# Performance work log

Hardware: AMD Instinct MI355X
Metric: run time of the kernel (lower is better)

The kernel has to match this reference:

```python
import jax, jax.numpy as jnp
import numpy as np

N = 8192
F_IN = 256
F_OUT = 64
ALPHA = 0.2  # LeakyReLU negative slope
MASK_VAL = -9e15


def setup_inputs() -> dict:
    key = jax.random.key(0)
    k1, k2, k3, k4 = jax.random.split(key, 4)
    h = jax.random.normal(k1, (N, F_IN), dtype=jnp.float32)
    adj = jax.random.randint(k2, (N, N), 0, 2, dtype=jnp.int32)  # 0/1 dense adjacency
    # Parameters (original creates them inside forward with xavier init; here fixed inputs)
    W = jax.random.normal(k3, (F_IN, F_OUT), dtype=jnp.float32) * (1.414 * np.sqrt(2.0 / (F_IN + F_OUT)))
    a = jax.random.normal(k4, (2 * F_OUT, 1), dtype=jnp.float32) * (1.414 * np.sqrt(2.0 / (2 * F_OUT + 1)))
    return {"h": h, "adj": adj, "W": W, "a": a}


def reference(h, adj, W, a):
    # Wh: [N, F_OUT]
    Wh = h @ W
    # e_ij = LeakyReLU(a^T [Wh_i ; Wh_j]) computed via broadcast instead of the
    f_src = Wh @ a[:F_OUT, 0]   # [N] contribution of row node i
    f_dst = Wh @ a[F_OUT:, 0]   # [N] contribution of col node j
    e = jax.nn.leaky_relu(f_src[:, None] + f_dst[None, :], negative_slope=ALPHA)  # [N, N]
    # adj-masked row softmax
    scores = jnp.where(adj > 0, e, MASK_VAL)
    attention = jax.nn.softmax(scores, axis=1)
    # dropout omitted (deterministic eval reference)
    h_prime = attention @ Wh  # [N, F_OUT]
    return jax.nn.elu(h_prime)  # concat=True branch
```

## Files before the change

kernel.cpp:

```cpp
#include <hip/hip_runtime.h>
#include <hip/hip_bf16.h>

#define NN 8192
#define FIN 256
#define FOUT 64
#define L2E 1.4426950408889634f
#define PADK 40

typedef __attribute__((ext_vector_type(8))) short short8;
typedef __attribute__((ext_vector_type(4))) float f32x4;
typedef __attribute__((ext_vector_type(4))) int   iv4;

#define BAR() do { \
  __asm__ __volatile__("s_waitcnt lgkmcnt(0)" ::: "memory"); \
  __builtin_amdgcn_s_barrier(); \
  __asm__ __volatile__("" ::: "memory"); \
} while (0)

__device__ __forceinline__ unsigned short f2bf(float x){
  unsigned u = __float_as_uint(x);
  u += 0x7FFFu + ((u >> 16) & 1u);
  return (unsigned short)(u >> 16);
}

__global__ __launch_bounds__(256) void k_pm(const float* __restrict__ h,
    const float* __restrict__ W, const float* __restrict__ a,
    const int* __restrict__ adj, unsigned short* __restrict__ WhT,
    float* __restrict__ fs, float* __restrict__ fd,
    unsigned* __restrict__ gmax_u, unsigned* __restrict__ mask){
  __shared__ float Ws[128*64];
  __shared__ float hs[8][128];
  const int bid = blockIdx.x, t = threadIdx.x;
  if (bid < 1024){
    const int l = t & 63, wv = t >> 6;
    const int rb = bid * 8;
    float acc0 = 0.f, acc1 = 0.f;
    for (int half = 0; half < 2; ++half){
      if (half) __syncthreads();
      for (int i = t; i < 2048; i += 256)
        ((float4*)Ws)[i] = ((const float4*)W)[half*2048 + i];
      {
        int rr = t >> 5, cc = t & 31;
        ((float4*)&hs[rr][0])[cc] =
            *(const float4*)(h + (size_t)(rb+rr)*FIN + half*128 + cc*4);
      }
      __syncthreads();
      #pragma unroll 8
      for (int k = 0; k < 128; ++k){
        float wval = Ws[k*64 + l];
        acc0 = fmaf(hs[wv*2+0][k], wval, acc0);
        acc1 = fmaf(hs[wv*2+1][k], wval, acc1);
      }
    }
    const int r0 = rb + wv*2, r1 = r0 + 1;
    float a1 = a[l], a2 = a[64 + l];
    float p0 = acc0*a1, q0 = acc0*a2, p1 = acc1*a1, q1 = acc1*a2;
    #pragma unroll
    for (int m = 1; m < 64; m <<= 1){
      p0 += __shfl_xor(p0, m); q0 += __shfl_xor(q0, m);
      p1 += __shfl_xor(p1, m); q1 += __shfl_xor(q1, m);
    }
    if (l == 0){
      fs[r0] = p0*L2E; fs[r1] = p1*L2E; fd[r0] = q0*L2E; fd[r1] = q1*L2E;
      atomicMax(gmax_u, __float_as_uint(q0*L2E + 64.0f));
      atomicMax(gmax_u, __float_as_uint(q1*L2E + 64.0f));
    }
    WhT[(size_t)l*NN + r0] = f2bf(acc0);
    WhT[(size_t)l*NN + r1] = f2bf(acc1);
  } else {
    unsigned char* nib = (unsigned char*)Ws;
    const unsigned b2 = (unsigned)(bid - 1024);
    #pragma unroll 1
    for (int it = 0; it < 16; ++it){
      const unsigned jb = (b2*16u + (unsigned)it) * 2048u;
      const iv4* p = (const iv4*)(adj + jb + (unsigned)t*8u);
      iv4 A = __builtin_nontemporal_load(p);
      iv4 B = __builtin_nontemporal_load(p + 1);
      unsigned by = (unsigned)(A.x!=0)        | ((unsigned)(A.y!=0)<<1)
                  | ((unsigned)(A.z!=0)<<2)   | ((unsigned)(A.w!=0)<<3)
                  | ((unsigned)(B.x!=0)<<4)   | ((unsigned)(B.y!=0)<<5)
                  | ((unsigned)(B.z!=0)<<6)   | ((unsigned)(B.w!=0)<<7);
      if (it) __syncthreads();
      nib[t] = (unsigned char)by;
      __syncthreads();
      if (t < 64) mask[(jb >> 5) + t] = ((const unsigned*)nib)[t];
    }
  }
}

__device__ __forceinline__ void attn_math(unsigned mbits, f32x4 fv0, f32x4 fv1,
    short8 w0, short8 w1, short8 w2, short8 w3,
    float fsrL, float mL, f32x4* acc, float& s0, float& s1){
  const float fv[8] = {fv0[0],fv0[1],fv0[2],fv0[3], fv1[0],fv1[1],fv1[2],fv1[3]};
  float w[8];
  #pragma unroll
  for (int j = 0; j < 8; ++j){
    float x  = fsrL + fv[j];
    float tt = fmaxf(x, 0.2f*x);
    float e  = __builtin_amdgcn_exp2f(tt - mL);
    w[j] = (mbits & (1u << j)) ? e : 0.0f;
  }
  s0 += (w[0]+w[2]) + (w[4]+w[6]);
  s1 += (w[1]+w[3]) + (w[5]+w[7]);
  short8 af;
  __hip_bfloat162* afp = (__hip_bfloat162*)&af;
  #pragma unroll
  for (int j = 0; j < 4; ++j)
    afp[j] = __float22bfloat162_rn(make_float2(w[2*j], w[2*j+1]));
  acc[0] = __builtin_amdgcn_mfma_f32_16x16x32_bf16(af, w0, acc[0], 0,0,0);
  acc[1] = __builtin_amdgcn_mfma_f32_16x16x32_bf16(af, w1, acc[1], 0,0,0);
  acc[2] = __builtin_amdgcn_mfma_f32_16x16x32_bf16(af, w2, acc[2], 0,0,0);
  acc[3] = __builtin_amdgcn_mfma_f32_16x16x32_bf16(af, w3, acc[3], 0,0,0);
}

__global__ __launch_bounds__(256, 4) void k_attn(const unsigned* __restrict__ mask,
    const unsigned short* __restrict__ WhT, const float* __restrict__ fs,
    const float* __restrict__ fd, const unsigned* __restrict__ gmax_u,
    float* __restrict__ acc_out, float* __restrict__ s_out){
  __shared__ unsigned short bslab[2][64*PADK];
  __shared__ float fslab[2][32];
  const int t = threadIdx.x, l = t & 63, wv = t >> 6;
  const int g = blockIdx.x & 127;
  const int kchunk = blockIdx.x >> 7;
  const int row = l & 15, quad = l >> 4;
  const int ibase = g*64 + wv*16;
  const int irow  = ibase + row;
  const float gmaxL = __uint_as_float(*gmax_u) - 64.0f;
  const float fsrL  = fs[irow];
  const float xL    = fsrL + gmaxL;
  const float mL    = fmaxf(xL, 0.2f*xL);

  const unsigned jbase = (unsigned)kchunk*1024u;
  const unsigned m_off = (unsigned)irow*256u + (jbase >> 5);
  const unsigned sg_off = (unsigned)l*8192u + jbase + (unsigned)wv*8u;
  const int      sl_off = l*PADK + wv*8;
  const int      qsh    = quad*8;

  f32x4 acc[4];
  #pragma unroll
  for (int nb = 0; nb < 4; ++nb) acc[nb] = (f32x4){0.f,0.f,0.f,0.f};

  {
    short8 v = *(const short8*)(WhT + sg_off);
    *(short8*)&bslab[0][sl_off] = v;
    if (t < 32) fslab[0][t] = fd[jbase + t];
  }
  unsigned m0 = mask[m_off + 0] >> qsh;
  unsigned m1 = mask[m_off + 1] >> qsh;

  float s0 = 0.f, s1 = 0.f;
  short8 nw; float nf = 0.f;

  #pragma unroll 1
  for (int s = 0; s < 32; s += 2){
    BAR();
    nw = *(const short8*)(WhT + sg_off + (s+1)*32);
    if (t < 32) nf = fd[jbase + (s+1)*32 + t];
    {
      f32x4 fv0 = *(const f32x4*)&fslab[0][qsh];
      f32x4 fv1 = *(const f32x4*)&fslab[0][qsh + 4];
      short8 w0 = *(const short8*)&bslab[0][( 0 + row)*PADK + qsh];
      short8 w1 = *(const short8*)&bslab[0][(16 + row)*PADK + qsh];
      short8 w2 = *(const short8*)&bslab[0][(32 + row)*PADK + qsh];
      short8 w3 = *(const short8*)&bslab[0][(48 + row)*PADK + qsh];
      attn_math(m0, fv0, fv1, w0, w1, w2, w3, fsrL, mL, acc, s0, s1);
    }
    if (s + 2 < 32) m0 = mask[m_off + s + 2] >> qsh;
    *(short8*)&bslab[1][sl_off] = nw;
    if (t < 32) fslab[1][t] = nf;

    BAR();
    if (s + 2 < 32){
      nw = *(const short8*)(WhT + sg_off + (s+2)*32);
      if (t < 32) nf = fd[jbase + (s+2)*32 + t];
    }
    {
      f32x4 fv0 = *(const f32x4*)&fslab[1][qsh];
      f32x4 fv1 = *(const f32x4*)&fslab[1][qsh + 4];
      short8 w0 = *(const short8*)&bslab[1][( 0 + row)*PADK + qsh];
      short8 w1 = *(const short8*)&bslab[1][(16 + row)*PADK + qsh];
      short8 w2 = *(const short8*)&bslab[1][(32 + row)*PADK + qsh];
      short8 w3 = *(const short8*)&bslab[1][(48 + row)*PADK + qsh];
      attn_math(m1, fv0, fv1, w0, w1, w2, w3, fsrL, mL, acc, s0, s1);
    }
    if (s + 3 < 32) m1 = mask[m_off + s + 3] >> qsh;
    if (s + 2 < 32){
      *(short8*)&bslab[0][sl_off] = nw;
      if (t < 32) fslab[0][t] = nf;
    }
  }

  float sacc = s0 + s1;
  sacc += __shfl_xor(sacc, 16);
  sacc += __shfl_xor(sacc, 32);
  if (l < 16) s_out[kchunk*NN + ibase + l] = sacc;
  float* op = acc_out + ((size_t)kchunk*NN + ibase)*FOUT;
  #pragma unroll
  for (int nb = 0; nb < 4; ++nb)
    #pragma unroll
    for (int r = 0; r < 4; ++r)
      op[(quad*4 + r)*FOUT + nb*16 + row] = acc[nb][r];
}

__global__ __launch_bounds__(256) void k_out(const float* __restrict__ acc,
    const float* __restrict__ s, float* __restrict__ out){
  const int idx = blockIdx.x*256 + threadIdx.x;
  const int i = idx >> 6;
  float num = 0.f, den = 0.f;
  #pragma unroll
  for (int ks = 0; ks < 8; ++ks){
    num += acc[idx + (size_t)ks*(NN*FOUT)];
    den += s[i + ks*NN];
  }
  float x = num / den;
  out[idx] = (x > 0.f) ? x : (__expf(x) - 1.0f);
}

extern "C" void kernel_launch(void* const* d_in, const int* in_sizes, int n_in,
                              void* d_out, int out_size, void* d_ws, size_t ws_size,
                              hipStream_t stream){
  const float* h   = (const float*)d_in[0];
  const int*   adj = (const int*)d_in[1];
  const float* W   = (const float*)d_in[2];
  const float* a   = (const float*)d_in[3];
  char* ws = (char*)d_ws;
  unsigned short* WhT = (unsigned short*)ws;
  float*    fs     = (float*)(ws + (1u<<20));
  float*    fd     = (float*)(ws + (1u<<20) + 32768);
  unsigned* gmax_u = (unsigned*)(ws + (1u<<20) + 65536);
  float*    acc    = (float*)(ws + (2u<<20));
  float*    s_ws   = (float*)(ws + (20u<<20));
  unsigned* mask   = (unsigned*)(ws + (48u<<20));

  (void)hipMemsetAsync(gmax_u, 0, 4, stream);
  k_pm<<<3072, 256, 0, stream>>>(h, W, a, adj, WhT, fs, fd, gmax_u, mask);
  k_attn<<<1024, 256, 0, stream>>>(mask, WhT, fs, fd, gmax_u, acc, s_ws);
  k_out<<<2048, 256, 0, stream>>>(acc, s_ws, (float*)d_out);
}
```

Before: 491.5 us.

## Pack adjacency bits per wave with ballots and interleave GEMM blocks

The adjacency-to-bitmask conversion now assigns one row per wave. Each wave issues eight outstanding 16-byte loads, packs the bits with four ballots plus a bit-spread, and writes the mask words directly, with no shared memory or block barriers. The Wh GEMM blocks are interleaved with conversion blocks (every third block) rather than grouped first, so compute and streaming blocks share the GPU at the same time. Loads switch from nontemporal to normal, which may change cache behaviour, and the ballot bit-shuffling adds some ALU work per load.

```diff
diff --git a/kernel.cpp b/kernel.cpp
--- a/kernel.cpp
+++ b/kernel.cpp
@@ -23,17 +23,44 @@
   return (unsigned short)(u >> 16);
 }
 
+__device__ __forceinline__ unsigned spread4(unsigned x){
+  x &= 0xFFu;
+  x = (x | (x << 12)) & 0x000F000Fu;
+  x = (x | (x << 6))  & 0x03030303u;
+  x = (x | (x << 3))  & 0x11111111u;
+  return x;
+}
+
+__device__ __forceinline__ void cv_process(iv4 d, int l,
+                                           unsigned* __restrict__ mp, int g){
+  unsigned n = (unsigned)(d.x != 0)        | ((unsigned)(d.y != 0) << 1)
+             | ((unsigned)(d.z != 0) << 2) | ((unsigned)(d.w != 0) << 3);
+  unsigned long long B0 = __ballot((n & 1u) != 0);
+  unsigned long long B1 = __ballot((n & 2u) != 0);
+  unsigned long long B2 = __ballot((n & 4u) != 0);
+  unsigned long long B3 = __ballot((n & 8u) != 0);
+  const int hi = l & 4, sh = (l & 3) * 8;
+  unsigned b0 = (unsigned)((hi ? (B0 >> 32) : B0) >> sh);
+  unsigned b1 = (unsigned)((hi ? (B1 >> 32) : B1) >> sh);
+  unsigned b2 = (unsigned)((hi ? (B2 >> 32) : B2) >> sh);
+  unsigned b3 = (unsigned)((hi ? (B3 >> 32) : B3) >> sh);
+  unsigned word = spread4(b0) | (spread4(b1) << 1)
+                | (spread4(b2) << 2) | (spread4(b3) << 3);
+  if (l < 8) mp[g*8 + l] = word;
+}
+
 __global__ __launch_bounds__(256) void k_pm(const float* __restrict__ h,
     const float* __restrict__ W, const float* __restrict__ a,
     const int* __restrict__ adj, unsigned short* __restrict__ WhT,
     float* __restrict__ fs, float* __restrict__ fd,
     unsigned* __restrict__ gmax_u, unsigned* __restrict__ mask){
-  __shared__ float Ws[128*64];
-  __shared__ float hs[8][128];
   const int bid = blockIdx.x, t = threadIdx.x;
-  if (bid < 1024){
-    const int l = t & 63, wv = t >> 6;
-    const int rb = bid * 8;
+  const int l = t & 63, wv = t >> 6;
+  if (bid % 3 == 0){
+    const int pid = bid / 3;
+    __shared__ float Ws[128*64];
+    __shared__ float hs[8][128];
+    const int rb = pid * 8;
     float acc0 = 0.f, acc1 = 0.f;
     for (int half = 0; half < 2; ++half){
       if (half) __syncthreads();
@@ -68,22 +95,22 @@
     WhT[(size_t)l*NN + r0] = f2bf(acc0);
     WhT[(size_t)l*NN + r1] = f2bf(acc1);
   } else {
-    unsigned char* nib = (unsigned char*)Ws;
-    const unsigned b2 = (unsigned)(bid - 1024);
+    const int cid = bid - bid/3 - 1;
+    const unsigned rowid = (unsigned)cid*4u + (unsigned)wv;
+    const iv4* __restrict__ ap = (const iv4*)(adj + (size_t)rowid*8192u) + l;
+    unsigned* __restrict__ mp = mask + rowid*256u;
+    iv4 d0 = ap[0*64], d1 = ap[1*64], d2 = ap[2*64], d3 = ap[3*64];
+    iv4 d4 = ap[4*64], d5 = ap[5*64], d6 = ap[6*64], d7 = ap[7*64];
     #pragma unroll 1
-    for (int it = 0; it < 16; ++it){
-      const unsigned jb = (b2*16u + (unsigned)it) * 2048u;
-      const iv4* p = (const iv4*)(adj + jb + (unsigned)t*8u);
-      iv4 A = __builtin_nontemporal_load(p);
-      iv4 B = __builtin_nontemporal_load(p + 1);
-      unsigned by = (unsigned)(A.x!=0)        | ((unsigned)(A.y!=0)<<1)
-                  | ((unsigned)(A.z!=0)<<2)   | ((unsigned)(A.w!=0)<<3)
-                  | ((unsigned)(B.x!=0)<<4)   | ((unsigned)(B.y!=0)<<5)
-                  | ((unsigned)(B.z!=0)<<6)   | ((unsigned)(B.w!=0)<<7);
-      if (it) __syncthreads();
-      nib[t] = (unsigned char)by;
-      __syncthreads();
-      if (t < 64) mask[(jb >> 5) + t] = ((const unsigned*)nib)[t];
+    for (int i = 0; i < 32; i += 8){
+      cv_process(d0, l, mp, i+0); if (i+ 8 < 32) d0 = ap[(i+ 8)*64];
+      cv_process(d1, l, mp, i+1); if (i+ 9 < 32) d1 = ap[(i+ 9)*64];
+      cv_process(d2, l, mp, i+2); if (i+10 < 32) d2 = ap[(i+10)*64];
+      cv_process(d3, l, mp, i+3); if (i+11 < 32) d3 = ap[(i+11)*64];
+      cv_process(d4, l, mp, i+4); if (i+12 < 32) d4 = ap[(i+12)*64];
+      cv_process(d5, l, mp, i+5); if (i+13 < 32) d5 = ap[(i+13)*64];
+      cv_process(d6, l, mp, i+6); if (i+14 < 32) d6 = ap[(i+14)*64];
+      cv_process(d7, l, mp, i+7); if (i+15 < 32) d7 = ap[(i+15)*64];
     }
   }
 }
```

Measured after the change: 444.6 us. 1.11x faster.
